# Kernel optimization log

Hardware: AMD Instinct MI355X
Metric: run time of the kernel (lower is better)

## Reference

```python
import jax, jax.numpy as jnp
import numpy as np

N, E, IN_DIM, OUT_DIM, SEM_DIM = 50000, 800000, 128, 128, 128
EPS = 1e-8


def setup_inputs() -> dict:
    key = jax.random.key(0)
    k = jax.random.split(key, 8)
    x = jax.random.normal(k[0], (N, IN_DIM), dtype=jnp.float32)
    edge_index = jax.random.randint(k[1], (2, E), 0, N, dtype=jnp.int64)
    semantic_vec = jax.random.normal(k[2], (N, SEM_DIM), dtype=jnp.float32)
    s = 1.0 / np.sqrt(IN_DIM)
    W_src = jax.random.uniform(k[3], (OUT_DIM, IN_DIM), jnp.float32, -s, s)
    b_src = jax.random.uniform(k[4], (OUT_DIM,), jnp.float32, -s, s)
    W_dst = jax.random.uniform(k[5], (OUT_DIM, IN_DIM), jnp.float32, -s, s)
    b_dst = jax.random.uniform(k[6], (OUT_DIM,), jnp.float32, -s, s)
    return {"x": x, "edge_index": edge_index, "semantic_vec": semantic_vec,
            "W_src": W_src, "b_src": b_src, "W_dst": W_dst, "b_dst": b_dst}


def _scatter_softmax(sim, dst, num_segments):
    # numerically stable segment-wise softmax over edges grouped by dst
    seg_max = jax.ops.segment_max(sim, dst, num_segments=num_segments)
    seg_max = jnp.where(jnp.isneginf(seg_max), 0.0, seg_max)
    e = jnp.exp(sim - seg_max[dst])
    seg_sum = jax.ops.segment_sum(e, dst, num_segments=num_segments)
    return e / (seg_sum[dst] + 1e-16)


def reference(x, edge_index, semantic_vec, W_src, b_src, W_dst, b_dst):
    src, dst = edge_index[0], edge_index[1]
    x_j = x[src] @ W_src.T + b_src           # [E, out_dim]
    # cosine similarity with torch eps semantics
    a = semantic_vec[src]
    b = semantic_vec[dst]
    na = jnp.maximum(jnp.linalg.norm(a, axis=-1), EPS)
    nb = jnp.maximum(jnp.linalg.norm(b, axis=-1), EPS)
    sim = jnp.sum(a * b, axis=-1) / (na * nb)  # [E]
    attn = _scatter_softmax(sim, dst, x.shape[0])
    msg = attn[:, None] * x_j                 # [E, out_dim]
    out = jax.ops.segment_sum(msg, dst, num_segments=x.shape[0])
    return out
```

## Files before the change

kernel.cpp:

```cpp
#include <hip/hip_runtime.h>
#include <hip/hip_fp16.h>

#define Nn 50000
#define Ee 800000
#define D  128
#define SLOT 64

#define NGRP 782
#define GRID_PRE (NGRP * 7)

typedef _Float16 f16x8 __attribute__((ext_vector_type(8)));
typedef _Float16 h2    __attribute__((ext_vector_type(2)));
typedef float    f32x4 __attribute__((ext_vector_type(4)));


__global__ __launch_bounds__(256) void k_zero(int* __restrict__ cnt) {
  int i = blockIdx.x * 256 + threadIdx.x;
  *(int4*)(cnt + i * 4) = (int4){0, 0, 0, 0};
}

__global__ __launch_bounds__(256, 8) void k_pre(const float* __restrict__ x,
                                                const float* __restrict__ W,
                                                const float* __restrict__ b,
                                                const int* __restrict__ ei,
                                                const float* __restrict__ sem,
                                                __half* __restrict__ blob,
                                                int* __restrict__ cnt,
                                                unsigned short* __restrict__ slot16) {
  int bid = blockIdx.x, tid = threadIdx.x;
  int nb = bid / 7, r = bid % 7;

  if (r == 0) {
    int base = nb * 1024 + tid;
#pragma unroll
    for (int u = 0; u < 4; u++) {
      int e = base + u * 256;
      if (e < Ee) {
        int s = ei[e], d = ei[Ee + e];
        int pos = atomicAdd(cnt + d, 1);
        if (pos < SLOT)
          slot16[(size_t)d * SLOT + pos] = (unsigned short)s;
      }
    }
  } else if (r <= 2) {
    int gb = nb * 2 + (r - 1);
    int n0 = gb * 32;
    int wave = tid >> 6, lane = tid & 63;
    int rs = (wave >> 1) * 16;
    int ch = (wave & 1) * 64;
    int g = lane >> 4, n16 = lane & 15;

    int arow = n0 + rs + n16; if (arow >= Nn) arow = Nn - 1;
    const float* xr = x + (size_t)arow * 128 + g * 8;
    union { f16x8 v; __half2 h[4]; } af[4];
#pragma unroll
    for (int kt = 0; kt < 4; kt++) {
      float4 u0 = *(const float4*)(xr + kt * 32);
      float4 u1 = *(const float4*)(xr + kt * 32 + 4);
      af[kt].h[0] = __floats2half2_rn(u0.x, u0.y);
      af[kt].h[1] = __floats2half2_rn(u0.z, u0.w);
      af[kt].h[2] = __floats2half2_rn(u1.x, u1.y);
      af[kt].h[3] = __floats2half2_rn(u1.z, u1.w);
    }

    f32x4 acc[4];
#pragma unroll
    for (int jt = 0; jt < 4; jt++) {
      float bias = b[ch + jt * 16 + n16];
      acc[jt] = (f32x4){bias, bias, bias, bias};
    }

    const float* wr = W + (size_t)(ch + n16) * 128 + g * 8;
#pragma unroll
    for (int kt = 0; kt < 4; kt++) {
#pragma unroll
      for (int jt = 0; jt < 4; jt++) {
        const float* wp = wr + (size_t)jt * 16 * 128 + kt * 32;
        float4 w0 = *(const float4*)(wp);
        float4 w1 = *(const float4*)(wp + 4);
        union { f16x8 v; __half2 h[4]; } bf;
        bf.h[0] = __floats2half2_rn(w0.x, w0.y);
        bf.h[1] = __floats2half2_rn(w0.z, w0.w);
        bf.h[2] = __floats2half2_rn(w1.x, w1.y);
        bf.h[3] = __floats2half2_rn(w1.z, w1.w);
        acc[jt] = __builtin_amdgcn_mfma_f32_16x16x32_f16(af[kt].v, bf.v, acc[jt], 0, 0, 0);
      }
    }
#pragma unroll
    for (int jt = 0; jt < 4; jt++) {
#pragma unroll
      for (int rr = 0; rr < 4; rr++) {
        int row = n0 + rs + g * 4 + rr;
        if (row < Nn)
          blob[(size_t)row * 256 + 128 + ch + jt * 16 + n16] = __float2half(acc[jt][rr]);
      }
    }
  } else {
    int idx = nb * 4 + (r - 3);
    int nb16 = idx * 16;
    int wave = tid >> 6, lane = tid & 63;
#pragma unroll
    for (int it = 0; it < 4; it++) {
      int n = nb16 + it * 4 + wave;
      if (n < Nn) {
        const float2 v = *(const float2*)(sem + (size_t)n * D + 2 * lane);
        float p = v.x * v.x + v.y * v.y;
#pragma unroll
        for (int off = 32; off > 0; off >>= 1) p += __shfl_xor(p, off);
        float inv = 1.0f / fmaxf(sqrtf(p), 1e-8f);
        *(__half2*)(blob + (size_t)n * 256 + 2 * lane) = __floats2half2_rn(v.x * inv, v.y * inv);
      }
    }
  }
}

__global__ __launch_bounds__(256) void k_fused(const __half* __restrict__ blob,
                                               const unsigned short* __restrict__ slot16,
                                               const int* __restrict__ cnt,
                                               float* __restrict__ out) {
  int d = (blockIdx.x * 256 + threadIdx.x) >> 6;
  int lane = threadIdx.x & 63;
  int g = lane >> 4, l16 = lane & 15;
  int c = cnt[d]; if (c > SLOT) c = SLOT;

  int sv = (lane < c) ? (int)slot16[(size_t)d * SLOT + lane] : 0;

  f16x8 dh = *(const f16x8*)(blob + (size_t)d * 256 + l16 * 8);

  float o[8] = {0, 0, 0, 0, 0, 0, 0, 0};
  float Sp = 0.0f;

  for (int i = 0; i < c; i += 4) {
    int e = i + g;
    int ce = e < c ? e : c - 1;
    int sa = __shfl(sv, ce);
    const __half* nbp = blob + (size_t)sa * 256;
    f16x8 rs = *(const f16x8*)(nbp + l16 * 8);
    f16x8 ry = *(const f16x8*)(nbp + 128 + l16 * 8);
    float p = __builtin_amdgcn_fdot2((h2){rs[0], rs[1]}, (h2){dh[0], dh[1]}, 0.0f, false);
    p = __builtin_amdgcn_fdot2((h2){rs[2], rs[3]}, (h2){dh[2], dh[3]}, p, false);
    p = __builtin_amdgcn_fdot2((h2){rs[4], rs[5]}, (h2){dh[4], dh[5]}, p, false);
    p = __builtin_amdgcn_fdot2((h2){rs[6], rs[7]}, (h2){dh[6], dh[7]}, p, false);
    p += __shfl_xor(p, 1); p += __shfl_xor(p, 2);
    p += __shfl_xor(p, 4); p += __shfl_xor(p, 8);
    float ew = __expf(p); if (e >= c) ew = 0.0f;
    Sp += ew;
#pragma unroll
    for (int k = 0; k < 8; k++) o[k] += ew * (float)ry[k];
  }

#pragma unroll
  for (int k = 0; k < 8; k++) {
    o[k] += __shfl_xor(o[k], 16);
    o[k] += __shfl_xor(o[k], 32);
  }
  Sp += __shfl_xor(Sp, 16);
  Sp += __shfl_xor(Sp, 32);

  if (g == 0) {
    float inv = 1.0f / (Sp + 1e-16f);
    float4 r0; r0.x = o[0] * inv; r0.y = o[1] * inv; r0.z = o[2] * inv; r0.w = o[3] * inv;
    float4 r1; r1.x = o[4] * inv; r1.y = o[5] * inv; r1.z = o[6] * inv; r1.w = o[7] * inv;
    float* op = out + (size_t)d * D + l16 * 8;
    *(float4*)op = r0;
    *(float4*)(op + 4) = r1;
  }
}

extern "C" void kernel_launch(void* const* d_in, const int* in_sizes, int n_in,
                              void* d_out, int out_size, void* d_ws, size_t ws_size,
                              hipStream_t stream) {
  const float* x     = (const float*)d_in[0];
  const int*   ei    = (const int*)d_in[1];
  const float* sem   = (const float*)d_in[2];
  const float* W_src = (const float*)d_in[3];
  const float* b_src = (const float*)d_in[4];
  float* out = (float*)d_out;

  char* ws = (char*)d_ws;
  const size_t O_BLOB = 0;
  const size_t O_CNT  = 25600000;
  const size_t O_SS   = 25804800;
  const size_t NEED   = 32204800;
  if (ws_size < NEED) return;

  __half* blob = (__half*)(ws + O_BLOB);
  int* cnt = (int*)(ws + O_CNT);
  unsigned short* slot16 = (unsigned short*)(ws + O_SS);

  k_zero<<<49, 256, 0, stream>>>(cnt);
  k_pre<<<GRID_PRE, 256, 0, stream>>>(x, W_src, b_src, ei, sem, blob, cnt, slot16);
  k_fused<<<(Nn + 3) / 4, 256, 0, stream>>>(blob, slot16, cnt, out);
}
```

Measured before the change: 229.6 us.

## Split fused pre-kernel into scatter and node kernels, stage W in LDS

The heterogeneous k_pre kernel, which mixed edge scatter, the node GEMM and semantic normalisation by block index, is split into two kernels. k_scat handles edge bucketing with vectorised int4 loads of the edge indices. k_node computes both the semantic normalisation and the x·W GEMM for 32 nodes per block, converting W once into padded fp16 shared memory instead of having every wave reload and convert W from global memory. This costs an extra kernel launch and serialises the scatter and node work that previously ran concurrently, and the 34KB of LDS per block may lower occupancy.

```diff
diff --git a/kernel.cpp b/kernel.cpp
--- a/kernel.cpp
+++ b/kernel.cpp
@@ -5,9 +5,6 @@
 #define Ee 800000
 #define D  128
 #define SLOT 64
-
-#define NGRP 782
-#define GRID_PRE (NGRP * 7)
 
 typedef _Float16 f16x8 __attribute__((ext_vector_type(8)));
 typedef _Float16 h2    __attribute__((ext_vector_type(2)));
@@ -19,97 +16,99 @@
   *(int4*)(cnt + i * 4) = (int4){0, 0, 0, 0};
 }
 
-__global__ __launch_bounds__(256, 8) void k_pre(const float* __restrict__ x,
-                                                const float* __restrict__ W,
-                                                const float* __restrict__ b,
-                                                const int* __restrict__ ei,
-                                                const float* __restrict__ sem,
-                                                __half* __restrict__ blob,
-                                                int* __restrict__ cnt,
-                                                unsigned short* __restrict__ slot16) {
+__global__ __launch_bounds__(256) void k_scat(const int* __restrict__ ei,
+                                              int* __restrict__ cnt,
+                                              unsigned short* __restrict__ slot16) {
+  int t = blockIdx.x * 256 + threadIdx.x;
+  int e0 = t * 4;
+  if (e0 >= Ee) return;
+  int4 s4 = *(const int4*)(ei + e0);
+  int4 d4 = *(const int4*)(ei + Ee + e0);
+  int ss[4] = {s4.x, s4.y, s4.z, s4.w};
+  int dd[4] = {d4.x, d4.y, d4.z, d4.w};
+#pragma unroll
+  for (int u = 0; u < 4; u++) {
+    int e = e0 + u;
+    if (e < Ee) {
+      int pos = atomicAdd(cnt + dd[u], 1);
+      if (pos < SLOT)
+        slot16[(size_t)dd[u] * SLOT + pos] = (unsigned short)ss[u];
+    }
+  }
+}
+
+__global__ __launch_bounds__(256) void k_node(const float* __restrict__ x,
+                                              const float* __restrict__ W,
+                                              const float* __restrict__ b,
+                                              const float* __restrict__ sem,
+                                              __half* __restrict__ blob) {
+  __shared__ __half sW16[128 * 136] __attribute__((aligned(16)));
   int bid = blockIdx.x, tid = threadIdx.x;
-  int nb = bid / 7, r = bid % 7;
+  int n0 = bid * 32;
+  int wave = tid >> 6, lane = tid & 63;
 
-  if (r == 0) {
-    int base = nb * 1024 + tid;
+  for (int r = 0; r < 16; r++) {
+    int i = tid + 256 * r;
+    int row = i >> 5, c4 = (i & 31) << 2;
+    float4 w = *(const float4*)(W + (size_t)row * 128 + c4);
+    __half2* dst = (__half2*)&sW16[row * 136 + c4];
+    dst[0] = __floats2half2_rn(w.x, w.y);
+    dst[1] = __floats2half2_rn(w.z, w.w);
+  }
+
 #pragma unroll
-    for (int u = 0; u < 4; u++) {
-      int e = base + u * 256;
-      if (e < Ee) {
-        int s = ei[e], d = ei[Ee + e];
-        int pos = atomicAdd(cnt + d, 1);
-        if (pos < SLOT)
-          slot16[(size_t)d * SLOT + pos] = (unsigned short)s;
-      }
+  for (int it = 0; it < 8; it++) {
+    int n = n0 + it * 4 + wave;
+    if (n < Nn) {
+      const float2 v = *(const float2*)(sem + (size_t)n * D + 2 * lane);
+      float p = v.x * v.x + v.y * v.y;
+#pragma unroll
+      for (int off = 32; off > 0; off >>= 1) p += __shfl_xor(p, off);
+      float inv = 1.0f / fmaxf(sqrtf(p), 1e-8f);
+      *(__half2*)(blob + (size_t)n * 256 + 2 * lane) = __floats2half2_rn(v.x * inv, v.y * inv);
     }
-  } else if (r <= 2) {
-    int gb = nb * 2 + (r - 1);
-    int n0 = gb * 32;
-    int wave = tid >> 6, lane = tid & 63;
-    int rs = (wave >> 1) * 16;
-    int ch = (wave & 1) * 64;
-    int g = lane >> 4, n16 = lane & 15;
+  }
 
-    int arow = n0 + rs + n16; if (arow >= Nn) arow = Nn - 1;
-    const float* xr = x + (size_t)arow * 128 + g * 8;
-    union { f16x8 v; __half2 h[4]; } af[4];
+  int rs = (wave >> 1) * 16;
+  int ch = (wave & 1) * 64;
+  int g = lane >> 4, n16 = lane & 15;
+
+  int arow = n0 + rs + n16; if (arow >= Nn) arow = Nn - 1;
+  const float* xr = x + (size_t)arow * 128 + g * 8;
+  union { f16x8 v; __half2 h[4]; } af[4];
 #pragma unroll
-    for (int kt = 0; kt < 4; kt++) {
-      float4 u0 = *(const float4*)(xr + kt * 32);
-      float4 u1 = *(const float4*)(xr + kt * 32 + 4);
-      af[kt].h[0] = __floats2half2_rn(u0.x, u0.y);
-      af[kt].h[1] = __floats2half2_rn(u0.z, u0.w);
-      af[kt].h[2] = __floats2half2_rn(u1.x, u1.y);
-      af[kt].h[3] = __floats2half2_rn(u1.z, u1.w);
-    }
+  for (int kt = 0; kt < 4; kt++) {
+    float4 u0 = *(const float4*)(xr + kt * 32);
+    float4 u1 = *(const float4*)(xr + kt * 32 + 4);
+    af[kt].h[0] = __floats2half2_rn(u0.x, u0.y);
+    af[kt].h[1] = __floats2half2_rn(u0.z, u0.w);
+    af[kt].h[2] = __floats2half2_rn(u1.x, u1.y);
+    af[kt].h[3] = __floats2half2_rn(u1.z, u1.w);
+  }
 
-    f32x4 acc[4];
+  __syncthreads();
+
+  f32x4 acc[4];
+#pragma unroll
+  for (int jt = 0; jt < 4; jt++) {
+    float bias = b[ch + jt * 16 + n16];
+    acc[jt] = (f32x4){bias, bias, bias, bias};
+  }
+#pragma unroll
+  for (int kt = 0; kt < 4; kt++) {
 #pragma unroll
     for (int jt = 0; jt < 4; jt++) {
-      float bias = b[ch + jt * 16 + n16];
-      acc[jt] = (f32x4){bias, bias, bias, bias};
+      f16x8 bf = *(const f16x8*)(&sW16[(ch + jt * 16 + n16) * 136 + kt * 32 + g * 8]);
+      acc[jt] = __builtin_amdgcn_mfma_f32_16x16x32_f16(af[kt].v, bf, acc[jt], 0, 0, 0);
     }
-
-    const float* wr = W + (size_t)(ch + n16) * 128 + g * 8;
+  }
 #pragma unroll
-    for (int kt = 0; kt < 4; kt++) {
+  for (int jt = 0; jt < 4; jt++) {
 #pragma unroll
-      for (int jt = 0; jt < 4; jt++) {
-        const float* wp = wr + (size_t)jt * 16 * 128 + kt * 32;
-        float4 w0 = *(const float4*)(wp);
-        float4 w1 = *(const float4*)(wp + 4);
-        union { f16x8 v; __half2 h[4]; } bf;
-        bf.h[0] = __floats2half2_rn(w0.x, w0.y);
-        bf.h[1] = __floats2half2_rn(w0.z, w0.w);
-        bf.h[2] = __floats2half2_rn(w1.x, w1.y);
-        bf.h[3] = __floats2half2_rn(w1.z, w1.w);
-        acc[jt] = __builtin_amdgcn_mfma_f32_16x16x32_f16(af[kt].v, bf.v, acc[jt], 0, 0, 0);
-      }
-    }
-#pragma unroll
-    for (int jt = 0; jt < 4; jt++) {
-#pragma unroll
-      for (int rr = 0; rr < 4; rr++) {
-        int row = n0 + rs + g * 4 + rr;
-        if (row < Nn)
-          blob[(size_t)row * 256 + 128 + ch + jt * 16 + n16] = __float2half(acc[jt][rr]);
-      }
-    }
-  } else {
-    int idx = nb * 4 + (r - 3);
-    int nb16 = idx * 16;
-    int wave = tid >> 6, lane = tid & 63;
-#pragma unroll
-    for (int it = 0; it < 4; it++) {
-      int n = nb16 + it * 4 + wave;
-      if (n < Nn) {
-        const float2 v = *(const float2*)(sem + (size_t)n * D + 2 * lane);
-        float p = v.x * v.x + v.y * v.y;
-#pragma unroll
-        for (int off = 32; off > 0; off >>= 1) p += __shfl_xor(p, off);
-        float inv = 1.0f / fmaxf(sqrtf(p), 1e-8f);
-        *(__half2*)(blob + (size_t)n * 256 + 2 * lane) = __floats2half2_rn(v.x * inv, v.y * inv);
-      }
+    for (int rr = 0; rr < 4; rr++) {
+      int row = n0 + rs + g * 4 + rr;
+      if (row < Nn)
+        blob[(size_t)row * 256 + 128 + ch + jt * 16 + n16] = __float2half(acc[jt][rr]);
     }
   }
 }
@@ -189,6 +188,7 @@
   unsigned short* slot16 = (unsigned short*)(ws + O_SS);
 
   k_zero<<<49, 256, 0, stream>>>(cnt);
-  k_pre<<<GRID_PRE, 256, 0, stream>>>(x, W_src, b_src, ei, sem, blob, cnt, slot16);
+  k_scat<<<782, 256, 0, stream>>>(ei, cnt, slot16);
+  k_node<<<1563, 256, 0, stream>>>(x, W_src, b_src, sem, blob);
   k_fused<<<(Nn + 3) / 4, 256, 0, stream>>>(blob, slot16, cnt, out);
 }
```

Result: faster. 217.5 us (-5.3%).
